# Kernel optimization log

Hardware: AMD Instinct MI355X
Metric: run time of the kernel (lower is better)

## Reference

```python
import jax, jax.numpy as jnp
import numpy as np

N_QUBITS = 18
BATCH = 64
NUM_LAYERS = 4


def setup_inputs() -> dict:
    key = jax.random.key(0)
    k1, k2 = jax.random.split(key)
    inputs = jax.random.normal(k1, (BATCH, N_QUBITS), dtype=jnp.float32)
    params = jax.random.normal(k2, (NUM_LAYERS, N_QUBITS, 1), dtype=jnp.float32)
    return {"inputs": inputs, "params": params}


def _apply_shared_1q(state, U, q, B):
    # state: (B, 2^n) complex; U: (2,2) complex; qubit q (wire 0 = most significant)
    st = state.reshape(B, 2 ** q, 2, -1)
    return jnp.einsum('ij,bxjy->bxiy', U, st).reshape(B, -1)


def _apply_batched_1q(state, U, q, B):
    # U: (B,2,2) complex, per-sample gate
    st = state.reshape(B, 2 ** q, 2, -1)
    return jnp.einsum('bij,bxjy->bxiy', U, st).reshape(B, -1)


def _apply_cnot(state, q, B):
    # control = q, target = q+1: flip target amplitudes where control == 1
    st = state.reshape(B, 2 ** q, 2, 2, -1)
    flipped = jnp.flip(st[:, :, 1], axis=2)  # (B, 2^q, 2, rest)
    st = jnp.concatenate([st[:, :, :1], flipped[:, :, None]], axis=2)
    return st.reshape(B, -1)


def reference(inputs, params):
    B, n = inputs.shape
    L = params.shape[0]
    state = jnp.zeros((B, 2 ** n), dtype=jnp.complex64).at[:, 0].set(1.0)

    # data-encoding RX(inputs[:, q]) on each qubit (per-sample angles)
    half = (inputs * 0.5).astype(jnp.float32)
    c = jnp.cos(half).astype(jnp.complex64)          # (B, n)
    s = (-1j * jnp.sin(half)).astype(jnp.complex64)  # (B, n)
    for q in range(n):
        U = jnp.stack([jnp.stack([c[:, q], s[:, q]], axis=-1),
                       jnp.stack([s[:, q], c[:, q]], axis=-1)], axis=-2)  # (B,2,2)
        state = _apply_batched_1q(state, U, q, B)

    # variational blocks: RY per qubit (shared angle) + CNOT ladder
    for layer in range(L):
        for q in range(n):
            th = params[layer, q, 0] * 0.5
            cc = jnp.cos(th).astype(jnp.complex64)
            ss = jnp.sin(th).astype(jnp.complex64)
            U = jnp.stack([jnp.stack([cc, -ss]), jnp.stack([ss, cc])])  # (2,2)
            state = _apply_shared_1q(state, U, q, B)
        for q in range(n - 1):
            state = _apply_cnot(state, q, B)
    return state
```

## Files before the change

kernel.cpp:

```cpp
#include <hip/hip_runtime.h>
#include <utility>

#define NQ 18
#define BATCH 64

#define VT_OFFC (1u << 24)
#define CS_OFFC (VT_OFFC + BATCH * NQ * 4)

__device__ __forceinline__ float2 cmulf(float2 a, float2 b) {
    return make_float2(a.x * b.x - a.y * b.y, a.x * b.y + a.y * b.x);
}

template<class F, int... Is>
__device__ __forceinline__ void unroll_impl(F f, std::integer_sequence<int, Is...>) {
    (f(std::integral_constant<int, Is>{}), ...);
}
template<int N, class F>
__device__ __forceinline__ void unroll(F f) {
    unroll_impl(f, std::make_integer_sequence<int, N>{});
}

struct Gate { int k, p; };
constexpr Gate GT[54] = {
    {2,13},{2,14},{2,15},{2,16},{2,17}, {3,14},{3,15},{3,16},{3,17}, {4,15},{4,16},{4,17},
    {2,11},{2,12}, {3,12},{3,13}, {4,13},{4,14},
    {2,8},{2,9},{2,10}, {3,9},{3,10},{3,11}, {4,10},{4,11},{4,12},
    {2,5},{2,6},{2,7}, {3,6},{3,7},{3,8}, {4,7},{4,8},{4,9},
    {2,0},{2,1},{2,2},{2,3},{2,4},
    {3,0},{3,1},{3,2},{3,3},{3,4},{3,5},
    {4,0},{4,1},{4,2},{4,3},{4,4},{4,5},{4,6},
};
constexpr unsigned gmask(Gate g) {
    return g.k == 2 ? (g.p >= 1 ? 3u << (g.p - 1) : 1u)
         : g.k == 3 ? (g.p >= 2 ? 5u << (g.p - 2) : 1u << g.p)
         : (g.p >= 3 ? 15u << (g.p - 3) : (1u << (g.p + 1)) - 1u);
}
constexpr unsigned gorient(Gate g) {
    return g.k == 2 ? (0x3FFFFu & ~((1u << g.p) - 1u))
         : g.k == 3 ? ((0x15555u << g.p) & 0x3FFFFu)
         : ((0x33333u << g.p) & 0x3FFFFu);
}
constexpr int gcsi(Gate g) { return (g.k - 2) * NQ + (17 - g.p); }

template<int WL, int OFF, int NG, int NR>
__device__ __forceinline__ void apply_gates(float* a, unsigned xfix, const float* csn) {
    unroll<NG>([&](auto I) {
        constexpr Gate g = GT[OFF + I.value];
        constexpr unsigned m  = gmask(g);
        constexpr unsigned O  = gorient(g);
        constexpr unsigned mr = (m >> WL) & (unsigned)(NR - 1);
        constexpr unsigned hb = 1u << (g.p - WL);
        constexpr unsigned Or = (O >> WL) & (unsigned)(NR - 1);
        constexpr unsigned Of = O & ~(((unsigned)(NR - 1)) << WL);
        float c = csn[2 * gcsi(g)], s = csn[2 * gcsi(g) + 1];
        float ps = (__popc(xfix & Of) & 1) ? -s : s;
        float ms = -ps;
        unroll<NR>([&](auto R) {
            constexpr int r = R.value;
            if constexpr ((r & (int)hb) == 0) {
                constexpr int r2 = r ^ (int)mr;
                constexpr bool fl = (__builtin_popcount((unsigned)r & Or) & 1) != 0;
                float se = fl ? ms : ps;
                float x0 = a[r], x1 = a[r2];
                a[r]  = c * x0 - se * x1;
                a[r2] = se * x0 + c * x1;
            }
        });
    });
}

__device__ __forceinline__ float4 perm4(float4 r, int k) {
    float t0 = r.x, t1 = r.y, t2 = r.z, t3 = r.w;
    if (k & 1) { float x; x=t0;t0=t1;t1=x; x=t2;t2=t3;t3=x; }
    if (k & 2) { float x; x=t0;t0=t2;t2=x; x=t1;t1=t3;t3=x; }
    return make_float4(t0, t1, t2, t3);
}

__global__ void k_prep(const float* __restrict__ inputs, const float* __restrict__ params,
                       float* __restrict__ ws) {
    int t = blockIdx.x * blockDim.x + threadIdx.x;
    if (t < BATCH * NQ) {
        int q = t % NQ;
        float x = 0.5f * inputs[t];
        float cx = cosf(x), sx = sinf(x);
        float th = 0.5f * params[q];
        float c = cosf(th), s = sinf(th);
        float* v = ws + VT_OFFC + t * 4;
        v[0] = c * cx;  v[1] = s * sx;
        v[2] = s * cx;  v[3] = -c * sx;
    } else if (t < BATCH * NQ + 54) {
        int i = t - BATCH * NQ;
        float th = 0.5f * params[NQ + i];
        ws[CS_OFFC + 2 * i]     = cosf(th);
        ws[CS_OFFC + 2 * i + 1] = sinf(th);
    }
}

__global__ __launch_bounds__(256) void k_passA(const float* __restrict__ ws_tab,
                                               float* __restrict__ ws) {
    __shared__ __align__(16) float lds[16384];
    const int b  = blockIdx.x >> 4;
    const int c4 = blockIdx.x & 15;
    const int t  = threadIdx.x;
    const float* vt  = ws_tab + VT_OFFC + b * NQ * 4;
    const float* csn = ws_tab + CS_OFFC;
    auto slot = [](unsigned y) { return y ^ ((y >> 6) & 31u); };

    unsigned xf0 = (unsigned)c4 | ((unsigned)t << 4);
    float2 pf = make_float2(1.f, 0.f);
    #pragma unroll
    for (int i = 0; i < 12; ++i) {
        int bit = (xf0 >> i) & 1;
        const float* vq = vt + (17 - i) * 4 + bit * 2;
        pf = cmulf(pf, make_float2(vq[0], vq[1]));
    }
    float2 ca[32];
    ca[0] = pf;
    #pragma unroll
    for (int bp = 0; bp < 5; ++bp) {
        const float* vq = vt + (5 - bp) * 4;
        float2 v0 = make_float2(vq[0], vq[1]), v1 = make_float2(vq[2], vq[3]);
        #pragma unroll
        for (int i = (1 << bp) - 1; i >= 0; --i) {
            float2 base = ca[i];
            ca[i + (1 << bp)] = cmulf(base, v1);
            ca[i] = cmulf(base, v0);
        }
    }
    float a[64];
    {
        const float* vq = vt;
        float2 v0 = make_float2(vq[0], vq[1]), v1 = make_float2(vq[2], vq[3]);
        #pragma unroll
        for (int i = 0; i < 32; ++i) {
            a[i]      = ca[i].x * v0.x - ca[i].y * v0.y;
            a[i + 32] = ca[i].x * v1.x - ca[i].y * v1.y;
        }
    }
    apply_gates<12, 0, 12, 64>(a, xf0, csn);

    #pragma unroll
    for (int j = 0; j < 64; ++j) lds[slot(((unsigned)j << 8) | (unsigned)t)] = a[j];
    __syncthreads();
    unsigned base1 = (unsigned)(t & 63) | ((unsigned)(t >> 6) << 12);
    #pragma unroll
    for (int j = 0; j < 64; ++j) a[j] = lds[slot(base1 | ((unsigned)j << 6))];
    unsigned xf1 = (unsigned)c4 | ((unsigned)(t & 63) << 4) | ((unsigned)(t >> 6) << 16);
    apply_gates<10, 12, 6, 64>(a, xf1, csn);
    #pragma unroll
    for (int j = 0; j < 64; ++j) lds[slot(base1 | ((unsigned)j << 6))] = a[j];
    __syncthreads();
    unsigned base2 = (unsigned)(t & 7) | ((unsigned)(t >> 3) << 9);
    #pragma unroll
    for (int j = 0; j < 64; ++j) a[j] = lds[slot(base2 | ((unsigned)j << 3))];
    unsigned xf2 = (unsigned)c4 | ((unsigned)(t & 7) << 4) | ((unsigned)(t >> 3) << 13);
    apply_gates<7, 18, 9, 64>(a, xf2, csn);
    #pragma unroll
    for (int j = 0; j < 64; ++j) lds[slot(base2 | ((unsigned)j << 3))] = a[j];
    __syncthreads();
    #pragma unroll
    for (int j = 0; j < 64; ++j) a[j] = lds[slot((unsigned)j | ((unsigned)t << 6))];
    unsigned xf3 = (unsigned)c4 | ((unsigned)t << 10);
    apply_gates<4, 27, 9, 64>(a, xf3, csn);

    float* wp = ws + (((size_t)b << 18) | ((size_t)(t >> 6) << 16)
                      | ((size_t)c4 << 9) | (size_t)(t & 63));
    unroll<64>([&](auto J) {
        constexpr int j = J.value;
        constexpr unsigned off = (unsigned)(((j >> 3) << 6) | ((j & 7) << 13));
        wp[off] = a[j];
    });
}

__global__ __launch_bounds__(256) void k_passB(const float* __restrict__ ws,
                                               float* __restrict__ out) {
    __shared__ __align__(16) float lds[16384];
    const int t = threadIdx.x;
    const int b = blockIdx.x >> 3;
    const int m = ((blockIdx.x & 7) << 8) | t;
    const float* csn = ws + CS_OFFC;
    unsigned Mv = (unsigned)m ^ ((unsigned)m >> 4);

    const float* rb = ws + (((size_t)b << 18)
                    | (size_t)((Mv >> 3) & 7u)
                    | ((size_t)((Mv >> 6) & 7u) << 3)
                    | ((size_t)(Mv & 7u) << 6)
                    | ((size_t)((Mv >> 9) & 3u) << 16));
    float a[128];
    unroll<128>([&](auto N) {
        constexpr int n = N.value;
        constexpr unsigned off = (unsigned)(((n & 15) << 9) | ((n >> 4) << 13));
        a[n] = rb[off];
    });
    apply_gates<0, 36, 18, 128>(a, Mv << 7, csn);

    unsigned cc = ((unsigned)m & 15u) << 3;
    float* obb = out + (((size_t)b << NQ) | ((size_t)(blockIdx.x & 7) << 15));
    const int w = t & 127;
    #pragma unroll
    for (int half = 0; half < 2; ++half) {
        if ((t >> 7) == half) {
            unroll<32>([&](auto Q) {
                constexpr int n0 = Q.value << 2;
                unsigned nx = (unsigned)n0 ^ cc;
                unsigned D  = (nx ^ (nx >> 4)) & 127u;
                unsigned Db = D & ~3u, kap = D & 3u;
                unsigned z0 = ((unsigned)w << 7) | Db;
                unsigned V  = (z0 >> 6) & 31u;
                unsigned Bq = z0 ^ (V & ~3u);
                float4 v = make_float4(a[n0], a[n0 ^ 1], a[n0 ^ 2], a[n0 ^ 3]);
                *(float4*)&lds[Bq] = perm4(v, (int)(kap ^ (V & 3u)));
            });
        }
        __syncthreads();
        float4* oh = (float4*)(obb + ((size_t)half << 14));
        int kp = (t >> 4) & 3;
        #pragma unroll
        for (int i = 0; i < 16; ++i) {
            unsigned f  = (unsigned)i * 256u + (unsigned)t;
            unsigned z0 = f << 2;
            unsigned V  = (z0 >> 6) & 31u;
            unsigned Bq = z0 ^ (V & ~3u);
            float4 r = *(const float4*)&lds[Bq];
            oh[f] = perm4(r, kp);
        }
        __syncthreads();
    }
}

__global__ __launch_bounds__(256) void k_init_f(const float* __restrict__ inputs,
                                                const float* __restrict__ params,
                                                float* __restrict__ S) {
    __shared__ float2 vt[2][NQ];
    int g = blockIdx.x * 256 + threadIdx.x;
    int b = g >> 13;
    int t = threadIdx.x;
    if (t < NQ) {
        float x = 0.5f * inputs[b * NQ + t];
        float cx = cosf(x), sx = sinf(x);
        float th = 0.5f * params[t];
        float c = cosf(th), s = sinf(th);
        vt[0][t] = make_float2(c * cx,  s * sx);
        vt[1][t] = make_float2(s * cx, -c * sx);
    }
    __syncthreads();
    unsigned OW = (unsigned)(g & 0x1FFF);
    unsigned iu = OW ^ (OW >> 1);
    int pu = OW & 1;
    float2 p = make_float2(1.f, 0.f);
    #pragma unroll
    for (int q = 0; q <= 12; ++q) {
        int bit = (iu >> (12 - q)) & 1;
        p = cmulf(p, vt[bit][q]);
    }
    float2 a[32];
    a[0] = p;
    #pragma unroll
    for (int bp = 0; bp < 5; ++bp) {
        float2 v0 = vt[0][17 - bp], v1 = vt[1][17 - bp];
        if (bp == 4 && pu) { float2 tt = v0; v0 = v1; v1 = tt; }
        #pragma unroll
        for (int i = (1 << bp) - 1; i >= 0; --i) {
            float2 base = a[i];
            a[i + (1 << bp)] = cmulf(base, v1);
            a[i] = cmulf(base, v0);
        }
    }
    float* outp = S + ((size_t)b << NQ) + ((size_t)OW << 5);
    #pragma unroll
    for (int oj = 0; oj < 32; oj += 4) {
        int k0 = oj ^ (oj >> 1);
        *(float4*)(outp + oj) = make_float4(a[k0].x, a[k0 ^ 1].x, a[k0 ^ 3].x, a[k0 ^ 2].x);
    }
}

template<int P>
__global__ __launch_bounds__(256) void k_pass_f(const float* __restrict__ params,
                                                float* __restrict__ S, int layer) {
    int g = blockIdx.x * 256 + threadIdx.x;
    float cg[6], sg[6];
    #pragma unroll
    for (int i = 0; i < 6; ++i) {
        float th = 0.5f * params[layer * NQ + 6 * P + i];
        cg[i] = cosf(th); sg[i] = sinf(th);
    }
    size_t base; int hm;
    constexpr int STR = (P == 0) ? 4096 : (P == 1) ? 64 : 1;
    if constexpr (P == 0) {
        base = ((size_t)(g >> 12) << NQ) | (size_t)(g & 0xFFF);
        hm = 0;
    } else if constexpr (P == 1) {
        base = ((size_t)(g >> 12) << NQ) | ((size_t)((g >> 6) & 63) << 12) | (size_t)(g & 63);
        hm = (g >> 6) & 1;
    } else {
        base = (size_t)g << 6;
        hm = g & 1;
    }
    float a[64];
    if constexpr (P == 2) {
        #pragma unroll
        for (int j = 0; j < 64; j += 4) {
            float4 w = *(const float4*)(S + base + j);
            a[j] = w.x; a[j + 1] = w.y; a[j + 2] = w.z; a[j + 3] = w.w;
        }
    } else {
        #pragma unroll
        for (int j = 0; j < 64; ++j) a[j] = S[base + (size_t)j * STR];
    }
    #pragma unroll
    for (int i = 0; i < 6; ++i) {
        int m = 32 >> i;
        #pragma unroll
        for (int r = 0; r < 64; ++r) if (!(r & m)) {
            float x0 = a[r], x1 = a[r | m];
            a[r]     = cg[i] * x0 - sg[i] * x1;
            a[r | m] = sg[i] * x0 + cg[i] * x1;
        }
    }
    if (hm) {
        #pragma unroll
        for (int r = 0; r < 32; ++r) { float tt = a[r]; a[r] = a[r ^ 32]; a[r ^ 32] = tt; }
    }
    if constexpr (P == 2) {
        #pragma unroll
        for (int oj = 0; oj < 64; oj += 4) {
            int k0 = oj ^ (oj >> 1);
            *(float4*)(S + base + oj) = make_float4(a[k0], a[k0 ^ 1], a[k0 ^ 3], a[k0 ^ 2]);
        }
    } else {
        #pragma unroll
        for (int oj = 0; oj < 64; ++oj)
            S[base + (size_t)oj * STR] = a[oj ^ (oj >> 1)];
    }
}

extern "C" void kernel_launch(void* const* d_in, const int* in_sizes, int n_in,
                              void* d_out, int out_size, void* d_ws, size_t ws_size,
                              hipStream_t stream) {
    const float* inputs = (const float*)d_in[0];
    const float* params = (const float*)d_in[1];
    float* out = (float*)d_out;
    float* ws  = (float*)d_ws;
    const size_t need = (size_t)4 * ((1ull << 24) + BATCH * NQ * 4 + 108);

    if (ws_size >= need) {
        k_prep<<<5, 256, 0, stream>>>(inputs, params, ws);
        k_passA<<<BATCH * 16, 256, 0, stream>>>(ws, ws);
        k_passB<<<512, 256, 0, stream>>>(ws, out);
    } else {
        k_init_f<<<2048, 256, 0, stream>>>(inputs, params, out);
        for (int layer = 1; layer < 4; ++layer) {
            k_pass_f<0><<<1024, 256, 0, stream>>>(params, out, layer);
            k_pass_f<1><<<1024, 256, 0, stream>>>(params, out, layer);
            k_pass_f<2><<<1024, 256, 0, stream>>>(params, out, layer);
        }
    }
}
```

Baseline: 94.23 us.

## Rework LDS swizzles in passA and halve passB LDS for occupancy

Replaces the generic slot() XOR swizzle in passA with per-stage swizzles whose constant parts fold into immediate offsets, so LDS addressing needs fewer runtime ops while avoiding bank conflicts. In passB the output transpose now goes through four quarter-sized rounds using a half-sized LDS buffer, with launch bounds asking for three blocks per CU. The readback drops the perm4 shuffle and moves the swizzle into the global store address. The extra rounds add barriers, and the occupancy hint may constrain register allocation for the 128-element register array.

```diff
diff --git a/kernel.cpp b/kernel.cpp
--- a/kernel.cpp
+++ b/kernel.cpp
@@ -104,7 +104,6 @@
     const int t  = threadIdx.x;
     const float* vt  = ws_tab + VT_OFFC + b * NQ * 4;
     const float* csn = ws_tab + CS_OFFC;
-    auto slot = [](unsigned y) { return y ^ ((y >> 6) & 31u); };
 
     unsigned xf0 = (unsigned)c4 | ((unsigned)t << 4);
     float2 pf = make_float2(1.f, 0.f);
@@ -139,27 +138,48 @@
     }
     apply_gates<12, 0, 12, 64>(a, xf0, csn);
 
-    #pragma unroll
-    for (int j = 0; j < 64; ++j) lds[slot(((unsigned)j << 8) | (unsigned)t)] = a[j];
+    unsigned St = (unsigned)t ^ ((unsigned)t >> 6);
+    unroll<8>([&](auto Rr) {
+        constexpr int r = Rr.value;
+        unsigned br = St ^ (unsigned)((r << 8) | (r << 2));
+        unroll<8>([&](auto Qq) {
+            constexpr int q = Qq.value;
+            lds[br + (q << 11)] = a[q * 8 + r];
+        });
+    });
     __syncthreads();
-    unsigned base1 = (unsigned)(t & 63) | ((unsigned)(t >> 6) << 12);
-    #pragma unroll
-    for (int j = 0; j < 64; ++j) a[j] = lds[slot(base1 | ((unsigned)j << 6))];
+
+    unsigned Sb1 = (unsigned)(t & 63) | ((unsigned)(t >> 6) << 12);
+    unroll<64>([&](auto J) {
+        constexpr unsigned K = (unsigned)((J.value << 6) | (J.value & 31));
+        a[J.value] = lds[Sb1 ^ K];
+    });
     unsigned xf1 = (unsigned)c4 | ((unsigned)(t & 63) << 4) | ((unsigned)(t >> 6) << 16);
     apply_gates<10, 12, 6, 64>(a, xf1, csn);
-    #pragma unroll
-    for (int j = 0; j < 64; ++j) lds[slot(base1 | ((unsigned)j << 6))] = a[j];
+    unroll<64>([&](auto J) {
+        constexpr unsigned K = (unsigned)((J.value << 6) | (J.value & 31));
+        lds[Sb1 ^ K] = a[J.value];
+    });
     __syncthreads();
-    unsigned base2 = (unsigned)(t & 7) | ((unsigned)(t >> 3) << 9);
-    #pragma unroll
-    for (int j = 0; j < 64; ++j) a[j] = lds[slot(base2 | ((unsigned)j << 3))];
+
+    unsigned Sb2 = ((unsigned)(t & 7) | ((unsigned)(t >> 3) << 9))
+                 ^ ((((unsigned)t >> 3) & 3u) << 3);
+    unroll<64>([&](auto J) {
+        constexpr unsigned K = (unsigned)((J.value << 3) | (J.value >> 3));
+        a[J.value] = lds[Sb2 ^ K];
+    });
     unsigned xf2 = (unsigned)c4 | ((unsigned)(t & 7) << 4) | ((unsigned)(t >> 3) << 13);
     apply_gates<7, 18, 9, 64>(a, xf2, csn);
-    #pragma unroll
-    for (int j = 0; j < 64; ++j) lds[slot(base2 | ((unsigned)j << 3))] = a[j];
+    unroll<64>([&](auto J) {
+        constexpr unsigned K = (unsigned)((J.value << 3) | (J.value >> 3));
+        lds[Sb2 ^ K] = a[J.value];
+    });
     __syncthreads();
-    #pragma unroll
-    for (int j = 0; j < 64; ++j) a[j] = lds[slot((unsigned)j | ((unsigned)t << 6))];
+
+    unsigned Sb3 = ((unsigned)t << 6) ^ ((unsigned)t & 31u);
+    unroll<64>([&](auto J) {
+        a[J.value] = lds[Sb3 ^ (unsigned)J.value];
+    });
     unsigned xf3 = (unsigned)c4 | ((unsigned)t << 10);
     apply_gates<4, 27, 9, 64>(a, xf3, csn);
 
@@ -172,9 +192,9 @@
     });
 }
 
-__global__ __launch_bounds__(256) void k_passB(const float* __restrict__ ws,
-                                               float* __restrict__ out) {
-    __shared__ __align__(16) float lds[16384];
+__global__ __launch_bounds__(256, 3) void k_passB(const float* __restrict__ ws,
+                                                  float* __restrict__ out) {
+    __shared__ __align__(16) float lds[8192];
     const int t = threadIdx.x;
     const int b = blockIdx.x >> 3;
     const int m = ((blockIdx.x & 7) << 8) | t;
@@ -196,34 +216,29 @@
 
     unsigned cc = ((unsigned)m & 15u) << 3;
     float* obb = out + (((size_t)b << NQ) | ((size_t)(blockIdx.x & 7) << 15));
-    const int w = t & 127;
-    #pragma unroll
-    for (int half = 0; half < 2; ++half) {
-        if ((t >> 7) == half) {
-            unroll<32>([&](auto Q) {
-                constexpr int n0 = Q.value << 2;
+    const unsigned w6 = (unsigned)(t & 63);
+    const unsigned Sw = (w6 << 7) ^ ((w6 << 1) & 28u);
+    const int myQ = t >> 6;
+    #pragma unroll
+    for (int Q = 0; Q < 4; ++Q) {
+        if (myQ == Q) {
+            unroll<32>([&](auto Qd) {
+                constexpr int n0 = Qd.value << 2;
                 unsigned nx = (unsigned)n0 ^ cc;
                 unsigned D  = (nx ^ (nx >> 4)) & 127u;
-                unsigned Db = D & ~3u, kap = D & 3u;
-                unsigned z0 = ((unsigned)w << 7) | Db;
-                unsigned V  = (z0 >> 6) & 31u;
-                unsigned Bq = z0 ^ (V & ~3u);
+                unsigned Bq = Sw ^ (D & ~3u);
                 float4 v = make_float4(a[n0], a[n0 ^ 1], a[n0 ^ 2], a[n0 ^ 3]);
-                *(float4*)&lds[Bq] = perm4(v, (int)(kap ^ (V & 3u)));
+                *(float4*)&lds[Bq] = perm4(v, (int)(D & 3u));
             });
         }
         __syncthreads();
-        float4* oh = (float4*)(obb + ((size_t)half << 14));
-        int kp = (t >> 4) & 3;
-        #pragma unroll
-        for (int i = 0; i < 16; ++i) {
-            unsigned f  = (unsigned)i * 256u + (unsigned)t;
-            unsigned z0 = f << 2;
-            unsigned V  = (z0 >> 6) & 31u;
-            unsigned Bq = z0 ^ (V & ~3u);
-            float4 r = *(const float4*)&lds[Bq];
-            oh[f] = perm4(r, kp);
-        }
+        float* ohQ = obb + ((size_t)Q << 13);
+        unroll<8>([&](auto I) {
+            constexpr int i = I.value;
+            unsigned p0 = ((unsigned)(i * 256) + (unsigned)t) << 2;
+            unsigned z0 = p0 ^ ((p0 >> 6) & 28u);
+            *(float4*)&ohQ[z0] = *(const float4*)&lds[p0];
+        });
         __syncthreads();
     }
 }
@@ -309,12 +324,12 @@
     }
     #pragma unroll
     for (int i = 0; i < 6; ++i) {
-        int m = 32 >> i;
-        #pragma unroll
-        for (int r = 0; r < 64; ++r) if (!(r & m)) {
-            float x0 = a[r], x1 = a[r | m];
-            a[r]     = cg[i] * x0 - sg[i] * x1;
-            a[r | m] = sg[i] * x0 + cg[i] * x1;
+        int mm = 32 >> i;
+        #pragma unroll
+        for (int r = 0; r < 64; ++r) if (!(r & mm)) {
+            float x0 = a[r], x1 = a[r | mm];
+            a[r]      = cg[i] * x0 - sg[i] * x1;
+            a[r | mm] = sg[i] * x0 + cg[i] * x1;
         }
     }
     if (hm) {
```

Result: slower. 108.2 us (+14.8%).
